# Kernel tuning notes

Measured on AMD Instinct MI355X. Metric: run time of the kernel, lower is better.

Reference implementation:

```python
import jax, jax.numpy as jnp
import numpy as np

B, S, D, H = 2, 2048, 1024, 16
DH = D // H
NEG = jnp.float32(-1e30)


def setup_inputs() -> dict:
    key = jax.random.key(0)
    ks = jax.random.split(key, 5)
    x = jax.random.normal(ks[0], (B, S, D), dtype=jnp.float32)
    # causal mask: attn_mask == 0 means blocked (matches masked_fill(attn_mask == 0))
    attn_mask = jnp.tril(jnp.ones((S, S), dtype=jnp.int32))
    key_padding_mask = jnp.zeros((B, S), dtype=bool)  # True = pad (none here)
    sd = 1.0 / np.sqrt(D)
    W_qkv = jax.random.normal(ks[1], (D, 3 * D), dtype=jnp.float32) * sd
    b_qkv = jnp.zeros((3 * D,), dtype=jnp.float32)
    W_proj = jax.random.normal(ks[2], (D, D), dtype=jnp.float32) * sd
    b_proj = jnp.zeros((D,), dtype=jnp.float32)
    return {"x": x, "W_qkv": W_qkv, "b_qkv": b_qkv, "W_proj": W_proj,
            "b_proj": b_proj, "attn_mask": attn_mask,
            "key_padding_mask": key_padding_mask}


def reference(x, W_qkv, b_qkv, W_proj, b_proj, attn_mask, key_padding_mask):
    scale = jnp.float32(DH) ** -0.5
    qkv = (x @ W_qkv + b_qkv).reshape(B, S, 3, H, DH)
    qkv = jnp.transpose(qkv, (2, 0, 3, 1, 4))  # (3, B, H, S, DH)
    q, k, v = qkv[0], qkv[1], qkv[2]
    attn = jnp.einsum("bhqd,bhkd->bhqk", q, k) * scale  # (B,H,S,S)
    # key padding mask: True -> -inf on that key column
    attn = jnp.where(key_padding_mask[:, None, None, :], NEG, attn)
    # attn mask: 0 -> blocked
    attn = jnp.where(attn_mask[None, None, :, :] == 0, NEG, attn)
    attn = jax.nn.softmax(attn, axis=-1)
    out = jnp.einsum("bhqk,bhkd->bhqd", attn, v)
    out = jnp.transpose(out, (0, 2, 1, 3)).reshape(B, S, D)
    return out @ W_proj + b_proj
```

## Files before the change

### kernel.cpp

```cpp
#include <hip/hip_runtime.h>


typedef __bf16 bf16;
typedef bf16 bf16x4 __attribute__((ext_vector_type(4)));
typedef bf16 bf16x8 __attribute__((ext_vector_type(8)));
typedef float f32x4 __attribute__((ext_vector_type(4)));

#define S_LEN 2048
#define DMODEL 1024
#define NHEAD 16
#define DHEAD 64

__device__ __forceinline__ void async_ld16(void* lds, const void* g) {
  __builtin_amdgcn_global_load_lds(
      (const __attribute__((address_space(1))) unsigned int*)g,
      (__attribute__((address_space(3))) unsigned int*)lds, 16, 0, 0);
}

__global__ __launch_bounds__(256) void prep_kernel(
    const float* __restrict__ x, const float* __restrict__ Wq,
    const float* __restrict__ Wp, bf16* __restrict__ Xb,
    bf16* __restrict__ Wtq, bf16* __restrict__ Wtp) {
  __shared__ float t[32][33];
  const int bid = blockIdx.x, tid = threadIdx.x;
  if (bid < 4096) {
    int i = bid * 256 + tid;
    float4 v = ((const float4*)x)[i];
    bf16x4 o;
    o[0] = (bf16)v.x; o[1] = (bf16)v.y; o[2] = (bf16)v.z; o[3] = (bf16)v.w;
    *(bf16x4*)(&Xb[4 * i]) = o;
    return;
  }
  const float* in; bf16* out; int R, C, bx, by;
  if (bid < 7168) {
    int b = bid - 4096; in = Wq; out = Wtq; R = 1024; C = 3072;
    bx = b % 96; by = b / 96;
  } else {
    int b = bid - 7168; in = Wp; out = Wtp; R = 1024; C = 1024;
    bx = b % 32; by = b / 32;
  }
  int tx = tid & 31, ty = tid >> 5;
  int bc = bx * 32, br = by * 32;
#pragma unroll
  for (int i = 0; i < 32; i += 8)
    t[ty + i][tx] = in[(size_t)(br + ty + i) * C + bc + tx];
  __syncthreads();
#pragma unroll
  for (int i = 0; i < 32; i += 8)
    out[(size_t)(bc + ty + i) * R + br + tx] = (bf16)t[tx][ty + i];
}

__global__ __launch_bounds__(256) void gemm_qkv(
    const bf16* __restrict__ A, const bf16* __restrict__ Bt,
    const float* __restrict__ bias, bf16* __restrict__ Oq,
    bf16* __restrict__ Ok, bf16* __restrict__ Ov, int Ksz) {
  __shared__ bf16 As[128 * 32];
  __shared__ bf16 Bs[128 * 32];
  const int tid = threadIdx.x, lane = tid & 63, w = tid >> 6;
  const int wm = (w >> 1) * 64, wn = (w & 1) * 64;
  const int lr = lane & 15, kg = lane >> 4;
  const int m0 = blockIdx.y * 128, n0 = blockIdx.x * 128;

  f32x4 acc[4][4] = {};

  for (int k0 = 0; k0 < Ksz; k0 += 32) {
#pragma unroll
    for (int i = 0; i < 2; ++i) {
      int seg = tid + i * 256;
      int row = seg >> 2, cs = (seg & 3) * 8;
      async_ld16(&As[row * 32 + cs], &A[(size_t)(m0 + row) * Ksz + k0 + cs]);
      async_ld16(&Bs[row * 32 + cs], &Bt[(size_t)(n0 + row) * Ksz + k0 + cs]);
    }
    __syncthreads();
    bf16x8 af[4], bfr[4];
#pragma unroll
    for (int i = 0; i < 4; ++i)
      af[i] = *(const bf16x8*)(&As[(wm + i * 16 + lr) * 32 + kg * 8]);
#pragma unroll
    for (int j = 0; j < 4; ++j)
      bfr[j] = *(const bf16x8*)(&Bs[(wn + j * 16 + lr) * 32 + kg * 8]);
#pragma unroll
    for (int i = 0; i < 4; ++i)
#pragma unroll
      for (int j = 0; j < 4; ++j)
        acc[i][j] = __builtin_amdgcn_mfma_f32_16x16x32_bf16(af[i], bfr[j], acc[i][j], 0, 0, 0);
    __syncthreads();
  }

  const int rbase = kg * 4;
#pragma unroll
  for (int i = 0; i < 4; ++i) {
#pragma unroll
    for (int j = 0; j < 4; ++j) {
      int ncol = n0 + wn + j * 16 + lr;
      float bv = bias[ncol];
#pragma unroll
      for (int r = 0; r < 4; ++r) {
        int m = m0 + wm + i * 16 + rbase + r;
        float v = acc[i][j][r] + bv;
        int t = ncol >> 10, rem = ncol & 1023;
        int h = rem >> 6, d = rem & 63;
        int s = m & 2047;
        size_t hb = (size_t)((m >> 11) * NHEAD + h) * S_LEN;
        if (t == 0)      Oq[(hb + s) * DHEAD + d] = (bf16)v;
        else if (t == 1) Ok[(hb + s) * DHEAD + d] = (bf16)v;
        else             Ov[hb * DHEAD + (size_t)d * S_LEN + s] = (bf16)v;
      }
    }
  }
}

__global__ __launch_bounds__(256) void gemm_proj(
    const bf16* __restrict__ A, const bf16* __restrict__ Bt,
    const float* __restrict__ bias, float* __restrict__ Of,
    int Ksz, int Nsz) {
  __shared__ bf16 As[64 * 32];
  __shared__ bf16 Bs[128 * 32];
  const int tid = threadIdx.x, lane = tid & 63, w = tid >> 6;
  const int wm = (w >> 1) * 32, wn = (w & 1) * 64;
  const int lr = lane & 15, kg = lane >> 4;
  const int m0 = blockIdx.y * 64, n0 = blockIdx.x * 128;

  f32x4 acc[2][4] = {};

  for (int k0 = 0; k0 < Ksz; k0 += 32) {
    {
      int row = tid >> 2, cs = (tid & 3) * 8;
      async_ld16(&As[row * 32 + cs], &A[(size_t)(m0 + row) * Ksz + k0 + cs]);
    }
#pragma unroll
    for (int i = 0; i < 2; ++i) {
      int seg = tid + i * 256;
      int row = seg >> 2, cs = (seg & 3) * 8;
      async_ld16(&Bs[row * 32 + cs], &Bt[(size_t)(n0 + row) * Ksz + k0 + cs]);
    }
    __syncthreads();
    bf16x8 af[2], bfr[4];
#pragma unroll
    for (int i = 0; i < 2; ++i)
      af[i] = *(const bf16x8*)(&As[(wm + i * 16 + lr) * 32 + kg * 8]);
#pragma unroll
    for (int j = 0; j < 4; ++j)
      bfr[j] = *(const bf16x8*)(&Bs[(wn + j * 16 + lr) * 32 + kg * 8]);
#pragma unroll
    for (int i = 0; i < 2; ++i)
#pragma unroll
      for (int j = 0; j < 4; ++j)
        acc[i][j] = __builtin_amdgcn_mfma_f32_16x16x32_bf16(af[i], bfr[j], acc[i][j], 0, 0, 0);
    __syncthreads();
  }

  const int rbase = kg * 4;
#pragma unroll
  for (int i = 0; i < 2; ++i) {
#pragma unroll
    for (int j = 0; j < 4; ++j) {
      int ncol = n0 + wn + j * 16 + lr;
      float bv = bias[ncol];
#pragma unroll
      for (int r = 0; r < 4; ++r) {
        int m = m0 + wm + i * 16 + rbase + r;
        Of[(size_t)m * Nsz + ncol] = acc[i][j][r] + bv;
      }
    }
  }
}

__global__ __launch_bounds__(256) void attn_kernel(
    const bf16* __restrict__ Q, const bf16* __restrict__ K,
    const bf16* __restrict__ Vtg, bf16* __restrict__ O) {
  __shared__ bf16 Ks[128 * 72];
  __shared__ bf16 Vt[80 * 136];
  __shared__ bf16 Pt[4][16 * 136];

  const int tid = threadIdx.x, lane = tid & 63, w = tid >> 6;
  const int lr = lane & 15, quad = lane >> 4;
  const int flat = blockIdx.x;
  const int p = (flat >> 3) & 15;
  const int bh = (flat & 7) + ((flat >> 7) << 3);
  const int b = bh >> 4, h = bh & 15;
  const bf16* Qp = Q + (size_t)bh * S_LEN * DHEAD;
  const bf16* Kp = K + (size_t)bh * S_LEN * DHEAD;
  const bf16* Vp = Vtg + (size_t)bh * S_LEN * DHEAD;

  for (int i = tid; i < 16 * 136; i += 256) {
    int rr = i / 136;
    Vt[(64 + rr) * 136 + (i - rr * 136)] = (rr == 0) ? (bf16)1.0f : (bf16)0.0f;
  }
  __syncthreads();

  const float qs = 0.125f * 1.44269504f;

  for (int seg = 0; seg < 2; ++seg) {
    const int qt = seg ? (31 - p) : p;
    const int q0 = qt * 64;
    const int qrow = q0 + w * 16;

    bf16x8 q0r = *(const bf16x8*)(Qp + (size_t)(qrow + lr) * DHEAD + quad * 8);
    bf16x8 q1r = *(const bf16x8*)(Qp + (size_t)(qrow + lr) * DHEAD + 32 + quad * 8);
    bf16x8 qf0, qf1;
#pragma unroll
    for (int e = 0; e < 8; ++e) {
      qf0[e] = (bf16)((float)q0r[e] * qs);
      qf1[e] = (bf16)((float)q1r[e] * qs);
    }

    f32x4 acc[4] = {};
    f32x4 acc5 = {};
    float m_i = -1e30f;

    const int ktiles = (q0 + 63) / 128 + 1;

    bf16x8 kreg[4], vreg[4];
#pragma unroll
    for (int i = 0; i < 4; ++i) {
      int sg = tid + i * 256;
      int krow = sg >> 3, kc = (sg & 7) * 8;
      kreg[i] = *(const bf16x8*)(&Kp[(size_t)krow * DHEAD + kc]);
      int vd = sg >> 4, vs = (sg & 15) * 8;
      vreg[i] = *(const bf16x8*)(&Vp[(size_t)vd * S_LEN + vs]);
    }

    for (int kt = 0; kt < ktiles; ++kt) {
      const int kb = kt * 128;
#pragma unroll
      for (int i = 0; i < 4; ++i) {
        int sg = tid + i * 256;
        int krow = sg >> 3, kc = (sg & 7) * 8;
        *(bf16x8*)(&Ks[krow * 72 + kc]) = kreg[i];
        int vd = sg >> 4, vs = (sg & 15) * 8;
        *(bf16x8*)(&Vt[vd * 136 + vs]) = vreg[i];
      }
      __syncthreads();

      if (kt + 1 < ktiles) {
        const int kbn = kb + 128;
#pragma unroll
        for (int i = 0; i < 4; ++i) {
          int sg = tid + i * 256;
          int krow = sg >> 3, kc = (sg & 7) * 8;
          kreg[i] = *(const bf16x8*)(&Kp[(size_t)(kbn + krow) * DHEAD + kc]);
          int vd = sg >> 4, vs = (sg & 15) * 8;
          vreg[i] = *(const bf16x8*)(&Vp[(size_t)vd * S_LEN + kbn + vs]);
        }
      }

      f32x4 sc[8];
      __builtin_amdgcn_s_setprio(1);
#pragma unroll
      for (int ct = 0; ct < 8; ++ct) {
        bf16x8 kf0 = *(const bf16x8*)(&Ks[(ct * 16 + lr) * 72 + quad * 8]);
        bf16x8 kf1 = *(const bf16x8*)(&Ks[(ct * 16 + lr) * 72 + 32 + quad * 8]);
        f32x4 a = {};
        a = __builtin_amdgcn_mfma_f32_16x16x32_bf16(kf0, qf0, a, 0, 0, 0);
        a = __builtin_amdgcn_mfma_f32_16x16x32_bf16(kf1, qf1, a, 0, 0, 0);
        sc[ct] = a;
      }
      __builtin_amdgcn_s_setprio(0);

      const bool full = (kb + 127) <= qrow;
      float pmax = -1e30f;
      if (full) {
#pragma unroll
        for (int ct = 0; ct < 8; ++ct)
#pragma unroll
          for (int r = 0; r < 4; ++r) pmax = fmaxf(pmax, sc[ct][r]);
      } else {
        const int qg = qrow + lr;
#pragma unroll
        for (int ct = 0; ct < 8; ++ct)
#pragma unroll
          for (int r = 0; r < 4; ++r) {
            int key = kb + ct * 16 + quad * 4 + r;
            if (key > qg) sc[ct][r] = -1e30f;
            pmax = fmaxf(pmax, sc[ct][r]);
          }
      }
      pmax = fmaxf(pmax, __shfl_xor(pmax, 16));
      pmax = fmaxf(pmax, __shfl_xor(pmax, 32));

      if (!__all(pmax <= m_i + 8.0f)) {
        float mn = fmaxf(m_i, pmax);
        float alpha = __builtin_amdgcn_exp2f(m_i - mn);
        m_i = mn;
#pragma unroll
        for (int nt = 0; nt < 4; ++nt)
#pragma unroll
          for (int r = 0; r < 4; ++r) acc[nt][r] *= alpha;
#pragma unroll
        for (int r = 0; r < 4; ++r) acc5[r] *= alpha;
      }

#pragma unroll
      for (int ct = 0; ct < 8; ++ct)
#pragma unroll
        for (int r = 0; r < 4; ++r)
          sc[ct][r] = __builtin_amdgcn_exp2f(sc[ct][r] - m_i);

#pragma unroll
      for (int ct = 0; ct < 8; ++ct) {
        bf16x4 pk;
#pragma unroll
        for (int r = 0; r < 4; ++r) pk[r] = (bf16)sc[ct][r];
        *(bf16x4*)(&Pt[w][lr * 136 + ct * 16 + quad * 4]) = pk;
      }

      __builtin_amdgcn_s_setprio(1);
#pragma unroll
      for (int k0 = 0; k0 < 4; ++k0) {
        bf16x8 pf = *(const bf16x8*)(&Pt[w][lr * 136 + k0 * 32 + quad * 8]);
#pragma unroll
        for (int nt = 0; nt < 4; ++nt) {
          bf16x8 vf = *(const bf16x8*)(&Vt[(nt * 16 + lr) * 136 + k0 * 32 + quad * 8]);
          acc[nt] = __builtin_amdgcn_mfma_f32_16x16x32_bf16(vf, pf, acc[nt], 0, 0, 0);
        }
        bf16x8 vf5 = *(const bf16x8*)(&Vt[(64 + lr) * 136 + k0 * 32 + quad * 8]);
        acc5 = __builtin_amdgcn_mfma_f32_16x16x32_bf16(vf5, pf, acc5, 0, 0, 0);
      }
      __builtin_amdgcn_s_setprio(0);
      __syncthreads();
    }

    float lsum = __shfl(acc5[0], lr);
    float inv = 1.f / lsum;
    size_t base = ((size_t)(b * S_LEN + qrow + lr)) * DMODEL + h * DHEAD;
#pragma unroll
    for (int nt = 0; nt < 4; ++nt) {
      bf16x4 ov;
#pragma unroll
      for (int r = 0; r < 4; ++r) ov[r] = (bf16)(acc[nt][r] * inv);
      *(bf16x4*)(&O[base + nt * 16 + quad * 4]) = ov;
    }
  }
}

extern "C" void kernel_launch(void* const* d_in, const int* in_sizes, int n_in,
                              void* d_out, int out_size, void* d_ws, size_t ws_size,
                              hipStream_t stream) {
  (void)in_sizes; (void)n_in; (void)out_size; (void)ws_size;
  const float* x     = (const float*)d_in[0];
  const float* Wqkv  = (const float*)d_in[1];
  const float* bqkv  = (const float*)d_in[2];
  const float* Wproj = (const float*)d_in[3];
  const float* bproj = (const float*)d_in[4];
  float* out = (float*)d_out;

  char* ws = (char*)d_ws;
  bf16* Xb  = (bf16*)(ws + 0);
  bf16* AO  = (bf16*)(ws + 0);
  bf16* Wtq = (bf16*)(ws + 8388608);
  bf16* Wtp = (bf16*)(ws + 16777216);
  bf16* Qb  = (bf16*)(ws + 18874368);
  bf16* Kb  = (bf16*)(ws + 27262976);
  bf16* Vtg = (bf16*)(ws + 35651584);

  prep_kernel<<<8192, 256, 0, stream>>>(x, Wqkv, Wproj, Xb, Wtq, Wtp);
  gemm_qkv<<<dim3(24, 32), 256, 0, stream>>>(Xb, Wtq, bqkv, Qb, Kb, Vtg, 1024);
  attn_kernel<<<512, 256, 0, stream>>>(Qb, Kb, Vtg, AO);
  gemm_proj<<<dim3(8, 64), 256, 0, stream>>>(AO, Wtp, bproj, out, 1024, 1024);
}
```

Measured before the change: 205.9 us.

## Double-buffer LDS tiles in QKV and projection GEMMs, vectorize V-transpose stores

```diff
diff --git a/kernel.cpp b/kernel.cpp
--- a/kernel.cpp
+++ b/kernel.cpp
@@ -54,8 +54,8 @@
     const bf16* __restrict__ A, const bf16* __restrict__ Bt,
     const float* __restrict__ bias, bf16* __restrict__ Oq,
     bf16* __restrict__ Ok, bf16* __restrict__ Ov, int Ksz) {
-  __shared__ bf16 As[128 * 32];
-  __shared__ bf16 Bs[128 * 32];
+  __shared__ bf16 As[2][128 * 32];
+  __shared__ bf16 Bs[2][128 * 32];
   const int tid = threadIdx.x, lane = tid & 63, w = tid >> 6;
   const int wm = (w >> 1) * 64, wn = (w & 1) * 64;
   const int lr = lane & 15, kg = lane >> 4;
@@ -63,48 +63,72 @@
 
   f32x4 acc[4][4] = {};
 
-  for (int k0 = 0; k0 < Ksz; k0 += 32) {
+  auto stage = [&](int buf, int k0) {
 #pragma unroll
     for (int i = 0; i < 2; ++i) {
       int seg = tid + i * 256;
       int row = seg >> 2, cs = (seg & 3) * 8;
-      async_ld16(&As[row * 32 + cs], &A[(size_t)(m0 + row) * Ksz + k0 + cs]);
-      async_ld16(&Bs[row * 32 + cs], &Bt[(size_t)(n0 + row) * Ksz + k0 + cs]);
-    }
-    __syncthreads();
+      async_ld16(&As[buf][row * 32 + cs], &A[(size_t)(m0 + row) * Ksz + k0 + cs]);
+      async_ld16(&Bs[buf][row * 32 + cs], &Bt[(size_t)(n0 + row) * Ksz + k0 + cs]);
+    }
+  };
+
+  stage(0, 0);
+  __syncthreads();
+  int cur = 0;
+  for (int k0 = 0; k0 < Ksz; k0 += 32) {
+    if (k0 + 32 < Ksz) stage(cur ^ 1, k0 + 32);
     bf16x8 af[4], bfr[4];
 #pragma unroll
     for (int i = 0; i < 4; ++i)
-      af[i] = *(const bf16x8*)(&As[(wm + i * 16 + lr) * 32 + kg * 8]);
+      af[i] = *(const bf16x8*)(&As[cur][(wm + i * 16 + lr) * 32 + kg * 8]);
 #pragma unroll
     for (int j = 0; j < 4; ++j)
-      bfr[j] = *(const bf16x8*)(&Bs[(wn + j * 16 + lr) * 32 + kg * 8]);
+      bfr[j] = *(const bf16x8*)(&Bs[cur][(wn + j * 16 + lr) * 32 + kg * 8]);
 #pragma unroll
     for (int i = 0; i < 4; ++i)
 #pragma unroll
       for (int j = 0; j < 4; ++j)
         acc[i][j] = __builtin_amdgcn_mfma_f32_16x16x32_bf16(af[i], bfr[j], acc[i][j], 0, 0, 0);
     __syncthreads();
+    cur ^= 1;
   }
 
   const int rbase = kg * 4;
-#pragma unroll
-  for (int i = 0; i < 4; ++i) {
-#pragma unroll
-    for (int j = 0; j < 4; ++j) {
-      int ncol = n0 + wn + j * 16 + lr;
-      float bv = bias[ncol];
-#pragma unroll
-      for (int r = 0; r < 4; ++r) {
-        int m = m0 + wm + i * 16 + rbase + r;
-        float v = acc[i][j][r] + bv;
-        int t = ncol >> 10, rem = ncol & 1023;
-        int h = rem >> 6, d = rem & 63;
+  const int t = n0 >> 10;
+  if (t == 2) {
+#pragma unroll
+    for (int i = 0; i < 4; ++i) {
+#pragma unroll
+      for (int j = 0; j < 4; ++j) {
+        int ncol = n0 + wn + j * 16 + lr;
+        float bv = bias[ncol];
+        int rem = ncol & 1023, h = rem >> 6, d = rem & 63;
+        int m = m0 + wm + i * 16 + rbase;
         int s = m & 2047;
         size_t hb = (size_t)((m >> 11) * NHEAD + h) * S_LEN;
-        if (t == 0)      Oq[(hb + s) * DHEAD + d] = (bf16)v;
-        else if (t == 1) Ok[(hb + s) * DHEAD + d] = (bf16)v;
-        else             Ov[hb * DHEAD + (size_t)d * S_LEN + s] = (bf16)v;
+        bf16x4 pk;
+#pragma unroll
+        for (int r = 0; r < 4; ++r) pk[r] = (bf16)(acc[i][j][r] + bv);
+        *(bf16x4*)(&Ov[hb * DHEAD + (size_t)d * S_LEN + s]) = pk;
+      }
+    }
+  } else {
+    bf16* Oqk = (t == 0) ? Oq : Ok;
+#pragma unroll
+    for (int i = 0; i < 4; ++i) {
+#pragma unroll
+      for (int j = 0; j < 4; ++j) {
+        int ncol = n0 + wn + j * 16 + lr;
+        float bv = bias[ncol];
+        int rem = ncol & 1023, h = rem >> 6, d = rem & 63;
+#pragma unroll
+        for (int r = 0; r < 4; ++r) {
+          int m = m0 + wm + i * 16 + rbase + r;
+          int s = m & 2047;
+          size_t hb = (size_t)((m >> 11) * NHEAD + h) * S_LEN;
+          Oqk[(hb + s) * DHEAD + d] = (bf16)(acc[i][j][r] + bv);
+        }
       }
     }
   }
@@ -114,8 +138,8 @@
     const bf16* __restrict__ A, const bf16* __restrict__ Bt,
     const float* __restrict__ bias, float* __restrict__ Of,
     int Ksz, int Nsz) {
-  __shared__ bf16 As[64 * 32];
-  __shared__ bf16 Bs[128 * 32];
+  __shared__ bf16 As[2][64 * 32];
+  __shared__ bf16 Bs[2][128 * 32];
   const int tid = threadIdx.x, lane = tid & 63, w = tid >> 6;
   const int wm = (w >> 1) * 32, wn = (w & 1) * 64;
   const int lr = lane & 15, kg = lane >> 4;
@@ -123,31 +147,38 @@
 
   f32x4 acc[2][4] = {};
 
-  for (int k0 = 0; k0 < Ksz; k0 += 32) {
+  auto stage = [&](int buf, int k0) {
     {
       int row = tid >> 2, cs = (tid & 3) * 8;
-      async_ld16(&As[row * 32 + cs], &A[(size_t)(m0 + row) * Ksz + k0 + cs]);
+      async_ld16(&As[buf][row * 32 + cs], &A[(size_t)(m0 + row) * Ksz + k0 + cs]);
     }
 #pragma unroll
     for (int i = 0; i < 2; ++i) {
       int seg = tid + i * 256;
       int row = seg >> 2, cs = (seg & 3) * 8;
-      async_ld16(&Bs[row * 32 + cs], &Bt[(size_t)(n0 + row) * Ksz + k0 + cs]);
-    }
-    __syncthreads();
+      async_ld16(&Bs[buf][row * 32 + cs], &Bt[(size_t)(n0 + row) * Ksz + k0 + cs]);
+    }
+  };
+
+  stage(0, 0);
+  __syncthreads();
+  int cur = 0;
+  for (int k0 = 0; k0 < Ksz; k0 += 32) {
+    if (k0 + 32 < Ksz) stage(cur ^ 1, k0 + 32);
     bf16x8 af[2], bfr[4];
 #pragma unroll
     for (int i = 0; i < 2; ++i)
-      af[i] = *(const bf16x8*)(&As[(wm + i * 16 + lr) * 32 + kg * 8]);
+      af[i] = *(const bf16x8*)(&As[cur][(wm + i * 16 + lr) * 32 + kg * 8]);
 #pragma unroll
     for (int j = 0; j < 4; ++j)
-      bfr[j] = *(const bf16x8*)(&Bs[(wn + j * 16 + lr) * 32 + kg * 8]);
+      bfr[j] = *(const bf16x8*)(&Bs[cur][(wn + j * 16 + lr) * 32 + kg * 8]);
 #pragma unroll
     for (int i = 0; i < 2; ++i)
 #pragma unroll
       for (int j = 0; j < 4; ++j)
         acc[i][j] = __builtin_amdgcn_mfma_f32_16x16x32_bf16(af[i], bfr[j], acc[i][j], 0, 0, 0);
     __syncthreads();
+    cur ^= 1;
   }
 
   const int rbase = kg * 4;
```

After: 212.9 us. +3.4%, slower.

## Register-prefetch GEMM tiles, enlarge QKV block to 256 rows, vectorize V-transpose stores

Applied to the files above, without the earlier changes.

```diff
diff --git a/kernel.cpp b/kernel.cpp
--- a/kernel.cpp
+++ b/kernel.cpp
@@ -50,28 +50,41 @@
     out[(size_t)(bc + ty + i) * R + br + tx] = (bf16)t[tx][ty + i];
 }
 
-__global__ __launch_bounds__(256) void gemm_qkv(
+__global__ __launch_bounds__(512) void gemm_qkv(
     const bf16* __restrict__ A, const bf16* __restrict__ Bt,
     const float* __restrict__ bias, bf16* __restrict__ Oq,
     bf16* __restrict__ Ok, bf16* __restrict__ Ov, int Ksz) {
-  __shared__ bf16 As[128 * 32];
+  __shared__ bf16 As[256 * 32];
   __shared__ bf16 Bs[128 * 32];
   const int tid = threadIdx.x, lane = tid & 63, w = tid >> 6;
   const int wm = (w >> 1) * 64, wn = (w & 1) * 64;
   const int lr = lane & 15, kg = lane >> 4;
-  const int m0 = blockIdx.y * 128, n0 = blockIdx.x * 128;
+  const int m0 = blockIdx.y * 256, n0 = blockIdx.x * 128;
 
   f32x4 acc[4][4] = {};
 
+  bf16x8 areg[2], breg;
+  const int ar0 = (tid) >> 2,        ac0 = (tid & 3) * 8;
+  const int ar1 = (tid + 512) >> 2,  ac1 = ((tid + 512) & 3) * 8;
+  const int br_ = tid >> 2,          bc_ = (tid & 3) * 8;
+
+  areg[0] = *(const bf16x8*)(&A[(size_t)(m0 + ar0) * Ksz + ac0]);
+  areg[1] = *(const bf16x8*)(&A[(size_t)(m0 + ar1) * Ksz + ac1]);
+  breg    = *(const bf16x8*)(&Bt[(size_t)(n0 + br_) * Ksz + bc_]);
+
   for (int k0 = 0; k0 < Ksz; k0 += 32) {
-#pragma unroll
-    for (int i = 0; i < 2; ++i) {
-      int seg = tid + i * 256;
-      int row = seg >> 2, cs = (seg & 3) * 8;
-      async_ld16(&As[row * 32 + cs], &A[(size_t)(m0 + row) * Ksz + k0 + cs]);
-      async_ld16(&Bs[row * 32 + cs], &Bt[(size_t)(n0 + row) * Ksz + k0 + cs]);
-    }
+    *(bf16x8*)(&As[ar0 * 32 + ac0]) = areg[0];
+    *(bf16x8*)(&As[ar1 * 32 + ac1]) = areg[1];
+    *(bf16x8*)(&Bs[br_ * 32 + bc_]) = breg;
     __syncthreads();
+
+    if (k0 + 32 < Ksz) {
+      const int kn = k0 + 32;
+      areg[0] = *(const bf16x8*)(&A[(size_t)(m0 + ar0) * Ksz + kn + ac0]);
+      areg[1] = *(const bf16x8*)(&A[(size_t)(m0 + ar1) * Ksz + kn + ac1]);
+      breg    = *(const bf16x8*)(&Bt[(size_t)(n0 + br_) * Ksz + kn + bc_]);
+    }
+
     bf16x8 af[4], bfr[4];
 #pragma unroll
     for (int i = 0; i < 4; ++i)
@@ -88,23 +101,40 @@
   }
 
   const int rbase = kg * 4;
-#pragma unroll
-  for (int i = 0; i < 4; ++i) {
-#pragma unroll
-    for (int j = 0; j < 4; ++j) {
-      int ncol = n0 + wn + j * 16 + lr;
-      float bv = bias[ncol];
-#pragma unroll
-      for (int r = 0; r < 4; ++r) {
-        int m = m0 + wm + i * 16 + rbase + r;
-        float v = acc[i][j][r] + bv;
-        int t = ncol >> 10, rem = ncol & 1023;
-        int h = rem >> 6, d = rem & 63;
+  const int t = n0 >> 10;
+  if (t == 2) {
+#pragma unroll
+    for (int i = 0; i < 4; ++i) {
+#pragma unroll
+      for (int j = 0; j < 4; ++j) {
+        int ncol = n0 + wn + j * 16 + lr;
+        float bv = bias[ncol];
+        int rem = ncol & 1023, h = rem >> 6, d = rem & 63;
+        int m = m0 + wm + i * 16 + rbase;
         int s = m & 2047;
         size_t hb = (size_t)((m >> 11) * NHEAD + h) * S_LEN;
-        if (t == 0)      Oq[(hb + s) * DHEAD + d] = (bf16)v;
-        else if (t == 1) Ok[(hb + s) * DHEAD + d] = (bf16)v;
-        else             Ov[hb * DHEAD + (size_t)d * S_LEN + s] = (bf16)v;
+        bf16x4 pk;
+#pragma unroll
+        for (int r = 0; r < 4; ++r) pk[r] = (bf16)(acc[i][j][r] + bv);
+        *(bf16x4*)(&Ov[hb * DHEAD + (size_t)d * S_LEN + s]) = pk;
+      }
+    }
+  } else {
+    bf16* Oqk = (t == 0) ? Oq : Ok;
+#pragma unroll
+    for (int i = 0; i < 4; ++i) {
+#pragma unroll
+      for (int j = 0; j < 4; ++j) {
+        int ncol = n0 + wn + j * 16 + lr;
+        float bv = bias[ncol];
+        int rem = ncol & 1023, h = rem >> 6, d = rem & 63;
+#pragma unroll
+        for (int r = 0; r < 4; ++r) {
+          int m = m0 + wm + i * 16 + rbase + r;
+          int s = m & 2047;
+          size_t hb = (size_t)((m >> 11) * NHEAD + h) * S_LEN;
+          Oqk[(hb + s) * DHEAD + d] = (bf16)(acc[i][j][r] + bv);
+        }
       }
     }
   }
@@ -123,18 +153,28 @@
 
   f32x4 acc[2][4] = {};
 
+  bf16x8 areg, breg[2];
+  const int ar_ = tid >> 2,          ac_ = (tid & 3) * 8;
+  const int br0 = tid >> 2,          bc0 = (tid & 3) * 8;
+  const int br1 = (tid + 256) >> 2,  bc1 = ((tid + 256) & 3) * 8;
+
+  areg    = *(const bf16x8*)(&A[(size_t)(m0 + ar_) * Ksz + ac_]);
+  breg[0] = *(const bf16x8*)(&Bt[(size_t)(n0 + br0) * Ksz + bc0]);
+  breg[1] = *(const bf16x8*)(&Bt[(size_t)(n0 + br1) * Ksz + bc1]);
+
   for (int k0 = 0; k0 < Ksz; k0 += 32) {
-    {
-      int row = tid >> 2, cs = (tid & 3) * 8;
-      async_ld16(&As[row * 32 + cs], &A[(size_t)(m0 + row) * Ksz + k0 + cs]);
-    }
-#pragma unroll
-    for (int i = 0; i < 2; ++i) {
-      int seg = tid + i * 256;
-      int row = seg >> 2, cs = (seg & 3) * 8;
-      async_ld16(&Bs[row * 32 + cs], &Bt[(size_t)(n0 + row) * Ksz + k0 + cs]);
-    }
+    *(bf16x8*)(&As[ar_ * 32 + ac_]) = areg;
+    *(bf16x8*)(&Bs[br0 * 32 + bc0]) = breg[0];
+    *(bf16x8*)(&Bs[br1 * 32 + bc1]) = breg[1];
     __syncthreads();
+
+    if (k0 + 32 < Ksz) {
+      const int kn = k0 + 32;
+      areg    = *(const bf16x8*)(&A[(size_t)(m0 + ar_) * Ksz + kn + ac_]);
+      breg[0] = *(const bf16x8*)(&Bt[(size_t)(n0 + br0) * Ksz + kn + bc0]);
+      breg[1] = *(const bf16x8*)(&Bt[(size_t)(n0 + br1) * Ksz + kn + bc1]);
+    }
+
     bf16x8 af[2], bfr[4];
 #pragma unroll
     for (int i = 0; i < 2; ++i)
@@ -355,7 +395,7 @@
   bf16* Vtg = (bf16*)(ws + 35651584);
 
   prep_kernel<<<8192, 256, 0, stream>>>(x, Wqkv, Wproj, Xb, Wtq, Wtp);
-  gemm_qkv<<<dim3(24, 32), 256, 0, stream>>>(Xb, Wtq, bqkv, Qb, Kb, Vtg, 1024);
+  gemm_qkv<<<dim3(24, 16), 512, 0, stream>>>(Xb, Wtq, bqkv, Qb, Kb, Vtg, 1024);
   attn_kernel<<<512, 256, 0, stream>>>(Qb, Kb, Vtg, AO);
   gemm_proj<<<dim3(8, 64), 256, 0, stream>>>(AO, Wtp, bproj, out, 1024, 1024);
 }
```

Measured after the change: 197.4 us. 1.04x faster.
